# Optimization experiments

Measured on AMD Instinct MI355X. Metric: run time of the kernel, lower is better.

Reference implementation:

```python
import jax, jax.numpy as jnp
import numpy as np

USER_NUM = 50000
ITEM_NUM = 50000
N = USER_NUM + ITEM_NUM
VT_DIM = 512
CAT_NUM = 1000
CAT_DIM = 32
HIDDEN = 128
OUT = 64
E = 2_000_000
BAG = 5


def setup_inputs() -> dict:
    key = jax.random.key(0)
    ks = jax.random.split(key, 12)
    inp = {
        "vt_feature": jax.random.normal(ks[0], (ITEM_NUM, VT_DIM), jnp.float32),
        "cat_indices": jax.random.randint(ks[1], (ITEM_NUM * BAG,), 0, CAT_NUM),
        "cat_offsets": jnp.arange(ITEM_NUM) * BAG,
        "edge_index": jax.random.randint(ks[2], (2, E), 0, N),
        # learned parameters
        "cat_table": jax.random.normal(ks[3], (CAT_NUM, CAT_DIM), jnp.float32) * 0.1,
        "fuse_w": jax.random.normal(ks[4], (HIDDEN, VT_DIM + CAT_DIM), jnp.float32) * (1.0 / np.sqrt(VT_DIM + CAT_DIM)),
        "user": jax.random.normal(ks[5], (USER_NUM, HIDDEN), jnp.float32) * 0.1,
        "w1_l": jax.random.normal(ks[6], (HIDDEN, HIDDEN), jnp.float32) * (1.0 / np.sqrt(HIDDEN)),
        "b1": jnp.zeros((HIDDEN,), jnp.float32),
        "w1_r": jax.random.normal(ks[7], (HIDDEN, HIDDEN), jnp.float32) * (1.0 / np.sqrt(HIDDEN)),
        "w2_l": jax.random.normal(ks[8], (OUT, HIDDEN), jnp.float32) * (1.0 / np.sqrt(HIDDEN)),
        "b2": jnp.zeros((OUT,), jnp.float32),
        "w2_r": jax.random.normal(ks[9], (OUT, HIDDEN), jnp.float32) * (1.0 / np.sqrt(HIDDEN)),
    }
    return inp


def _embedding_bag_mean(table, indices, offsets, num_bags):
    # EmbeddingBag(mode='mean') with offsets: segment-mean of table lookups.
    pos = jnp.arange(indices.shape[0])
    seg = jnp.searchsorted(offsets, pos, side="right") - 1  # bag id per index
    sums = jax.ops.segment_sum(table[indices], seg, num_segments=num_bags)
    cnt = jax.ops.segment_sum(jnp.ones_like(pos, jnp.float32), seg, num_segments=num_bags)
    return sums / jnp.maximum(cnt, 1.0)[:, None]


def _sage_conv(x, edge_index, w_l, b_l, w_r):
    # PyG SAGEConv (aggr='mean'): lin_l(mean_{j->i} x_j) + lin_r(x_i)
    src, dst = edge_index[0], edge_index[1]
    agg = jax.ops.segment_sum(x[src], dst, num_segments=N)
    deg = jax.ops.segment_sum(jnp.ones((src.shape[0],), x.dtype), dst, num_segments=N)
    agg = agg / jnp.maximum(deg, 1.0)[:, None]
    return agg @ w_l.T + b_l + x @ w_r.T


def reference(vt_feature, cat_indices, cat_offsets, edge_index, cat_table,
              fuse_w, user, w1_l, b1, w1_r, w2_l, b2, w2_r):
    cat_emb = _embedding_bag_mean(cat_table, cat_indices, cat_offsets, ITEM_NUM)
    item_feat = jnp.concatenate([vt_feature, cat_emb], axis=1) @ fuse_w.T
    x0 = jnp.concatenate([user, item_feat], axis=0)  # [N, hidden]
    x1 = jax.nn.leaky_relu(_sage_conv(x0, edge_index, w1_l, b1, w1_r), negative_slope=0.01)
    # dropout is identity in eval mode
    x2 = _sage_conv(x1, edge_index, w2_l, b2, w2_r)
    return x2
```

## Files before the change

### kernel.cpp

```cpp
#include <hip/hip_runtime.h>

#define USER_N   50000
#define ITEM_N   50000
#define NNODE    100000
#define VT_DIM   512
#define CAT_DIM  32
#define HIDDEN   128
#define OUTD     64
#define PADCAP   64

#define BINC    8192
#define NBKT    98
#define BSHIFT  10
#define SLICES  8

typedef __attribute__((ext_vector_type(8))) short short8;
typedef __attribute__((ext_vector_type(4))) float f32x4;

__device__ __forceinline__ float bf2f(unsigned short u) {
    return __uint_as_float(((unsigned int)u) << 16);
}
__device__ __forceinline__ unsigned short f2bf(float f) {
    unsigned int u = __float_as_uint(f);
    unsigned int r = u + 0x7fffu + ((u >> 16) & 1u);
    return (unsigned short)(r >> 16);
}
__device__ __forceinline__ unsigned int pk2(float lo, float hi) {
    return ((unsigned int)f2bf(hi) << 16) | (unsigned int)f2bf(lo);
}
__device__ __forceinline__ void acc8(float* a, uint4 v) {
    a[0] += __uint_as_float(v.x << 16);
    a[1] += __uint_as_float(v.x & 0xffff0000u);
    a[2] += __uint_as_float(v.y << 16);
    a[3] += __uint_as_float(v.y & 0xffff0000u);
    a[4] += __uint_as_float(v.z << 16);
    a[5] += __uint_as_float(v.z & 0xffff0000u);
    a[6] += __uint_as_float(v.w << 16);
    a[7] += __uint_as_float(v.w & 0xffff0000u);
}
__device__ __forceinline__ void acc8w(float* a, uint4 v, float w) {
    a[0] += w * __uint_as_float(v.x << 16);
    a[1] += w * __uint_as_float(v.x & 0xffff0000u);
    a[2] += w * __uint_as_float(v.y << 16);
    a[3] += w * __uint_as_float(v.y & 0xffff0000u);
    a[4] += w * __uint_as_float(v.z << 16);
    a[5] += w * __uint_as_float(v.z & 0xffff0000u);
    a[6] += w * __uint_as_float(v.w << 16);
    a[7] += w * __uint_as_float(v.w & 0xffff0000u);
}

__global__ __launch_bounds__(256) void k_catemb(const float* __restrict__ cat_table,
                                                const int* __restrict__ cat_idx,
                                                const int* __restrict__ cat_off,
                                                unsigned short* __restrict__ catemb,
                                                int item_num, int total_idx) {
    int gid = blockIdx.x * 256 + threadIdx.x;
    int item = gid >> 5;
    int d = gid & 31;
    if (item >= item_num) return;
    int s = cat_off[item];
    int e = (item + 1 < item_num) ? cat_off[item + 1] : total_idx;
    float acc = 0.f;
    for (int j = s; j < e; ++j) {
        int idx = cat_idx[j];
        acc += cat_table[idx * CAT_DIM + d];
    }
    int cnt = e - s;
    float inv = 1.f / (float)(cnt > 0 ? cnt : 1);
    catemb[(size_t)item * CAT_DIM + d] = f2bf(acc * inv);
}

__global__ __launch_bounds__(256) void k_copy_user(const float* __restrict__ user,
                                                   unsigned short* __restrict__ x0, int n4) {
    int gid = blockIdx.x * 256 + threadIdx.x;
    if (gid >= n4) return;
    float4 v = ((const float4*)user)[gid];
    ushort4 o;
    o.x = f2bf(v.x); o.y = f2bf(v.y); o.z = f2bf(v.z); o.w = f2bf(v.w);
    ((ushort4*)x0)[gid] = o;
}

#define ASTR 40

__global__ __launch_bounds__(256, 4) void k_fuse_mfma(const float* __restrict__ vt,
                                                      const unsigned short* __restrict__ catemb,
                                                      const float* __restrict__ fw,
                                                      unsigned short* __restrict__ x0) {
    __shared__ __align__(16) unsigned short Al[64 * ASTR];
    __shared__ __align__(16) unsigned short Bl[128 * ASTR];
    int tid = threadIdx.x;
    int wave = tid >> 6, lane = tid & 63, quad = lane >> 4, l16 = lane & 15;
    int br0 = blockIdx.x * 64;
    int row = tid >> 2, q4 = tid & 3;
    int arow = br0 + row;

    f32x4 acc[8];
#pragma unroll
    for (int n = 0; n < 8; n++) acc[n] = (f32x4){0.f, 0.f, 0.f, 0.f};

    for (int kb = 0; kb < 17; ++kb) {
        if (kb < 16) {
            if (arow < ITEM_N) {
                const float* src = vt + (size_t)arow * VT_DIM + kb * 32 + q4 * 8;
                float4 v0 = ((const float4*)src)[0];
                float4 v1 = ((const float4*)src)[1];
                ushort4 o0, o1;
                o0.x = f2bf(v0.x); o0.y = f2bf(v0.y); o0.z = f2bf(v0.z); o0.w = f2bf(v0.w);
                o1.x = f2bf(v1.x); o1.y = f2bf(v1.y); o1.z = f2bf(v1.z); o1.w = f2bf(v1.w);
                *(ushort4*)&Al[row * ASTR + q4 * 8]     = o0;
                *(ushort4*)&Al[row * ASTR + q4 * 8 + 4] = o1;
            } else {
                ushort4 z = {0, 0, 0, 0};
                *(ushort4*)&Al[row * ASTR + q4 * 8]     = z;
                *(ushort4*)&Al[row * ASTR + q4 * 8 + 4] = z;
            }
        } else {
            if (arow < ITEM_N) {
                uint4 v = *(const uint4*)(catemb + (size_t)arow * CAT_DIM + q4 * 8);
                *(uint4*)&Al[row * ASTR + q4 * 8] = v;
            } else {
                uint4 z = {0, 0, 0, 0};
                *(uint4*)&Al[row * ASTR + q4 * 8] = z;
            }
        }
        {
            int n = tid & 127, kh = tid >> 7;
            const float* src = fw + (size_t)n * (VT_DIM + CAT_DIM) + kb * 32 + kh * 16;
#pragma unroll
            for (int i = 0; i < 4; i++) {
                float4 v = ((const float4*)src)[i];
                ushort4 o;
                o.x = f2bf(v.x); o.y = f2bf(v.y); o.z = f2bf(v.z); o.w = f2bf(v.w);
                *(ushort4*)&Bl[n * ASTR + kh * 16 + i * 4] = o;
            }
        }
        __syncthreads();
        short8 av = *(const short8*)&Al[(wave * 16 + l16) * ASTR + quad * 8];
#pragma unroll
        for (int nf = 0; nf < 8; nf++) {
            short8 bv = *(const short8*)&Bl[(nf * 16 + l16) * ASTR + quad * 8];
            acc[nf] = __builtin_amdgcn_mfma_f32_16x16x32_bf16(av, bv, acc[nf], 0, 0, 0);
        }
        __syncthreads();
    }
    int rbase = br0 + wave * 16 + quad * 4;
#pragma unroll
    for (int r = 0; r < 4; r++) {
        int orow = rbase + r;
        if (orow < ITEM_N) {
#pragma unroll
            for (int nf = 0; nf < 8; nf++) {
                int col = nf * 16 + l16;
                x0[(size_t)(USER_N + orow) * HIDDEN + col] = f2bf(acc[nf][r]);
            }
        }
    }
}

__global__ __launch_bounds__(256, 4) void k_l1_mfma(const unsigned short* __restrict__ agg1,
                                                    const unsigned short* __restrict__ x0,
                                                    const float* __restrict__ w1l,
                                                    const float* __restrict__ w1r,
                                                    const float* __restrict__ b1,
                                                    unsigned short* __restrict__ x1) {
    __shared__ __align__(16) unsigned short Al[64 * ASTR];
    __shared__ __align__(16) unsigned short Bl[128 * ASTR];
    int tid = threadIdx.x;
    int wave = tid >> 6, lane = tid & 63, quad = lane >> 4, l16 = lane & 15;
    int br0 = blockIdx.x * 64;
    int row = tid >> 2, q4 = tid & 3;
    int arow = br0 + row;

    f32x4 acc[8];
#pragma unroll
    for (int n = 0; n < 8; n++) acc[n] = (f32x4){0.f, 0.f, 0.f, 0.f};

    for (int kb = 0; kb < 8; ++kb) {
        const unsigned short* abase = (kb < 4) ? agg1 : x0;
        int kc = (kb & 3) * 32;
        if (arow < NNODE) {
            uint4 v = *(const uint4*)(abase + (size_t)arow * HIDDEN + kc + q4 * 8);
            *(uint4*)&Al[row * ASTR + q4 * 8] = v;
        } else {
            uint4 z = {0, 0, 0, 0};
            *(uint4*)&Al[row * ASTR + q4 * 8] = z;
        }
        {
            int n = tid & 127, kh = tid >> 7;
            const float* src = ((kb < 4) ? w1l : w1r) + (size_t)n * HIDDEN + kc + kh * 16;
#pragma unroll
            for (int i = 0; i < 4; i++) {
                float4 v = ((const float4*)src)[i];
                ushort4 o;
                o.x = f2bf(v.x); o.y = f2bf(v.y); o.z = f2bf(v.z); o.w = f2bf(v.w);
                *(ushort4*)&Bl[n * ASTR + kh * 16 + i * 4] = o;
            }
        }
        __syncthreads();
        short8 av = *(const short8*)&Al[(wave * 16 + l16) * ASTR + quad * 8];
#pragma unroll
        for (int nf = 0; nf < 8; nf++) {
            short8 bv = *(const short8*)&Bl[(nf * 16 + l16) * ASTR + quad * 8];
            acc[nf] = __builtin_amdgcn_mfma_f32_16x16x32_bf16(av, bv, acc[nf], 0, 0, 0);
        }
        __syncthreads();
    }
    float bias[8];
#pragma unroll
    for (int nf = 0; nf < 8; nf++) bias[nf] = b1[nf * 16 + l16];
    int rbase = br0 + wave * 16 + quad * 4;
#pragma unroll
    for (int r = 0; r < 4; r++) {
        int orow = rbase + r;
        if (orow < NNODE) {
#pragma unroll
            for (int nf = 0; nf < 8; nf++) {
                int col = nf * 16 + l16;
                float v = acc[nf][r] + bias[nf];
                v = (v >= 0.f) ? v : 0.01f * v;
                x1[(size_t)orow * HIDDEN + col] = f2bf(v);
            }
        }
    }
}

__global__ __launch_bounds__(256, 4) void k_l2_mfma(const unsigned short* __restrict__ x1,
                                                    const float* __restrict__ w2l,
                                                    const float* __restrict__ w2r,
                                                    const float* __restrict__ b2,
                                                    unsigned short* __restrict__ y1,
                                                    float* __restrict__ outw) {
    __shared__ __align__(16) unsigned short Al[64 * ASTR];
    __shared__ __align__(16) unsigned short Bl[128 * ASTR];
    int tid = threadIdx.x;
    int wave = tid >> 6, lane = tid & 63, quad = lane >> 4, l16 = lane & 15;
    int br0 = blockIdx.x * 64;
    int row = tid >> 2, q4 = tid & 3;
    int arow = br0 + row;

    f32x4 acc[8];
#pragma unroll
    for (int n = 0; n < 8; n++) acc[n] = (f32x4){0.f, 0.f, 0.f, 0.f};

    for (int kb = 0; kb < 4; ++kb) {
        int kc = kb * 32;
        if (arow < NNODE) {
            uint4 v = *(const uint4*)(x1 + (size_t)arow * HIDDEN + kc + q4 * 8);
            *(uint4*)&Al[row * ASTR + q4 * 8] = v;
        } else {
            uint4 z = {0, 0, 0, 0};
            *(uint4*)&Al[row * ASTR + q4 * 8] = z;
        }
        {
            int n = tid & 127, kh = tid >> 7;
            const float* wsrc = (n < 64) ? (w2l + (size_t)n * HIDDEN)
                                         : (w2r + (size_t)(n - 64) * HIDDEN);
            const float* src = wsrc + kc + kh * 16;
#pragma unroll
            for (int i = 0; i < 4; i++) {
                float4 v = ((const float4*)src)[i];
                ushort4 o;
                o.x = f2bf(v.x); o.y = f2bf(v.y); o.z = f2bf(v.z); o.w = f2bf(v.w);
                *(ushort4*)&Bl[n * ASTR + kh * 16 + i * 4] = o;
            }
        }
        __syncthreads();
        short8 av = *(const short8*)&Al[(wave * 16 + l16) * ASTR + quad * 8];
#pragma unroll
        for (int nf = 0; nf < 8; nf++) {
            short8 bv = *(const short8*)&Bl[(nf * 16 + l16) * ASTR + quad * 8];
            acc[nf] = __builtin_amdgcn_mfma_f32_16x16x32_bf16(av, bv, acc[nf], 0, 0, 0);
        }
        __syncthreads();
    }
    float bias2[4];
#pragma unroll
    for (int nf = 0; nf < 4; nf++) bias2[nf] = b2[nf * 16 + l16];
    int rbase = br0 + wave * 16 + quad * 4;
#pragma unroll
    for (int r = 0; r < 4; r++) {
        int orow = rbase + r;
        if (orow < NNODE) {
#pragma unroll
            for (int nf = 0; nf < 4; nf++) {
                int col = nf * 16 + l16;
                y1[(size_t)orow * OUTD + col] = f2bf(acc[nf][r]);
            }
#pragma unroll
            for (int nf = 4; nf < 8; nf++) {
                int col = (nf - 4) * 16 + l16;
                outw[(size_t)orow * OUTD + col] = acc[nf][r] + bias2[nf - 4];
            }
        }
    }
}

__global__ __launch_bounds__(256) void k_deg(const int* __restrict__ dst, int ne4, int ne, int* __restrict__ deg) {
    int t = blockIdx.x * 256 + threadIdx.x;
    int base = t * 4;
    if (t < ne4) {
        int4 d4 = *(const int4*)&dst[base];
        atomicAdd(&deg[d4.x], 1);
        atomicAdd(&deg[d4.y], 1);
        atomicAdd(&deg[d4.z], 1);
        atomicAdd(&deg[d4.w], 1);
    } else {
        for (int e = base; e < ne; ++e) atomicAdd(&deg[dst[e]], 1);
    }
}

__global__ __launch_bounds__(256) void k_scanA(const int* __restrict__ deg, int n, int* __restrict__ bsum) {
    __shared__ int sd[256];
    int i = blockIdx.x * 256 + threadIdx.x;
    sd[threadIdx.x] = (i < n) ? deg[i] : 0;
    __syncthreads();
    for (int o = 128; o > 0; o >>= 1) {
        if (threadIdx.x < o) sd[threadIdx.x] += sd[threadIdx.x + o];
        __syncthreads();
    }
    if (threadIdx.x == 0) bsum[blockIdx.x] = sd[0];
}

__global__ __launch_bounds__(512) void k_scanB(const int* __restrict__ bsum, int nb, int* __restrict__ boff) {
    __shared__ int sd[512];
    int t = threadIdx.x;
    int v = (t < nb) ? bsum[t] : 0;
    sd[t] = v;
    __syncthreads();
    for (int o = 1; o < 512; o <<= 1) {
        int x = 0;
        if (t >= o) x = sd[t - o];
        __syncthreads();
        sd[t] += x;
        __syncthreads();
    }
    if (t < nb) boff[t] = sd[t] - v;
}

__global__ __launch_bounds__(256) void k_scanC(const int* __restrict__ deg, int n,
                                               const int* __restrict__ boff,
                                               int* __restrict__ offs, int* __restrict__ cursor, int ne) {
    __shared__ int sd[256];
    int i = blockIdx.x * 256 + threadIdx.x;
    int v = (i < n) ? deg[i] : 0;
    sd[threadIdx.x] = v;
    __syncthreads();
    for (int o = 1; o < 256; o <<= 1) {
        int x = 0;
        if (threadIdx.x >= o) x = sd[threadIdx.x - o];
        __syncthreads();
        sd[threadIdx.x] += x;
        __syncthreads();
    }
    if (i < n) {
        int ex = boff[blockIdx.x] + sd[threadIdx.x] - v;
        offs[i] = ex;
        cursor[i] = ex;
    }
    if (i == 0) offs[n] = ne;
}

__global__ __launch_bounds__(256) void k_scatter(const int* __restrict__ src, const int* __restrict__ dst,
                                                 int ne4, int ne, int* __restrict__ cursor, int* __restrict__ csr) {
    int t = blockIdx.x * 256 + threadIdx.x;
    int base = t * 4;
    if (t < ne4) {
        int4 d4 = *(const int4*)&dst[base];
        int4 s4 = *(const int4*)&src[base];
        int p0 = atomicAdd(&cursor[d4.x], 1);
        int p1 = atomicAdd(&cursor[d4.y], 1);
        int p2 = atomicAdd(&cursor[d4.z], 1);
        int p3 = atomicAdd(&cursor[d4.w], 1);
        csr[p0] = s4.x;
        csr[p1] = s4.y;
        csr[p2] = s4.z;
        csr[p3] = s4.w;
    } else {
        for (int e = base; e < ne; ++e) {
            int slot = atomicAdd(&cursor[dst[e]], 1);
            csr[slot] = src[e];
        }
    }
}

__global__ __launch_bounds__(256) void k_scatter_pad(const int* __restrict__ src, const int* __restrict__ dst,
                                                     int ne4, int ne, int* __restrict__ cursor,
                                                     int* __restrict__ csrp) {
    int t = blockIdx.x * 256 + threadIdx.x;
    int base = t * 4;
    if (t < ne4) {
        int4 d4 = *(const int4*)&dst[base];
        int4 s4 = *(const int4*)&src[base];
        int p0 = atomicAdd(&cursor[d4.x], 1);
        int p1 = atomicAdd(&cursor[d4.y], 1);
        int p2 = atomicAdd(&cursor[d4.z], 1);
        int p3 = atomicAdd(&cursor[d4.w], 1);
        if (p0 < PADCAP) csrp[d4.x * PADCAP + p0] = s4.x;
        if (p1 < PADCAP) csrp[d4.y * PADCAP + p1] = s4.y;
        if (p2 < PADCAP) csrp[d4.z * PADCAP + p2] = s4.z;
        if (p3 < PADCAP) csrp[d4.w * PADCAP + p3] = s4.w;
    } else {
        for (int e = base; e < ne; ++e) {
            int d = dst[e];
            int slot = atomicAdd(&cursor[d], 1);
            if (slot < PADCAP) csrp[d * PADCAP + slot] = src[e];
        }
    }
}

__global__ __launch_bounds__(256) void k_hist(const int* __restrict__ dst, int ne,
                                              int nblk, int* __restrict__ hist) {
    __shared__ int lh[NBKT];
    int b = blockIdx.x;
    for (int i = threadIdx.x; i < NBKT; i += 256) lh[i] = 0;
    __syncthreads();
    int s = b * BINC;
    int e = (s + BINC < ne) ? (s + BINC) : ne;
    int nv = (e - s) & ~3;
    for (int j = s + threadIdx.x * 4; j < s + nv; j += 1024) {
        int4 d4 = *(const int4*)&dst[j];
        atomicAdd(&lh[d4.x >> BSHIFT], 1);
        atomicAdd(&lh[d4.y >> BSHIFT], 1);
        atomicAdd(&lh[d4.z >> BSHIFT], 1);
        atomicAdd(&lh[d4.w >> BSHIFT], 1);
    }
    for (int j = s + nv + threadIdx.x; j < e; j += 256) {
        atomicAdd(&lh[dst[j] >> BSHIFT], 1);
    }
    __syncthreads();
    for (int i = threadIdx.x; i < NBKT; i += 256) hist[i * nblk + b] = lh[i];
}

__global__ __launch_bounds__(1024) void k_scan1(int* __restrict__ hist, int tot) {
    __shared__ int ls[1024];
    int t = threadIdx.x;
    int K = (tot + 1023) >> 10;
    int base = t * K;
    int end = base + K;
    if (end > tot) end = tot;
    int s = 0;
    for (int i = base; i < end; ++i) s += hist[i];
    ls[t] = s;
    __syncthreads();
    for (int o = 1; o < 1024; o <<= 1) {
        int v = (t >= o) ? ls[t - o] : 0;
        __syncthreads();
        ls[t] += v;
        __syncthreads();
    }
    int run = ls[t] - s;
    for (int i = base; i < end; ++i) {
        int tmp = hist[i];
        hist[i] = run;
        run += tmp;
    }
}

__global__ __launch_bounds__(256) void k_binscatter(const int* __restrict__ src,
                                                    const int* __restrict__ dst,
                                                    int ne, int nblk,
                                                    const int* __restrict__ hist,
                                                    int2* __restrict__ ebin) {
    __shared__ int lc[NBKT];
    int b = blockIdx.x;
    for (int i = threadIdx.x; i < NBKT; i += 256) lc[i] = hist[i * nblk + b];
    __syncthreads();
    int s = b * BINC;
    int e = (s + BINC < ne) ? (s + BINC) : ne;
    int nv = (e - s) & ~3;
    for (int j = s + threadIdx.x * 4; j < s + nv; j += 1024) {
        int4 d4 = *(const int4*)&dst[j];
        int4 s4 = *(const int4*)&src[j];
        int p0 = atomicAdd(&lc[d4.x >> BSHIFT], 1);
        int p1 = atomicAdd(&lc[d4.y >> BSHIFT], 1);
        int p2 = atomicAdd(&lc[d4.z >> BSHIFT], 1);
        int p3 = atomicAdd(&lc[d4.w >> BSHIFT], 1);
        ebin[p0] = make_int2(s4.x, d4.x);
        ebin[p1] = make_int2(s4.y, d4.y);
        ebin[p2] = make_int2(s4.z, d4.z);
        ebin[p3] = make_int2(s4.w, d4.w);
    }
    for (int j = s + nv + threadIdx.x; j < e; j += 256) {
        int d = dst[j];
        int p = atomicAdd(&lc[d >> BSHIFT], 1);
        ebin[p] = make_int2(src[j], d);
    }
}

__global__ __launch_bounds__(256) void k_scatter_bkt(const int2* __restrict__ ebin,
                                                     const int* __restrict__ hist,
                                                     int nblk, int ne,
                                                     int* __restrict__ cursor,
                                                     int* __restrict__ csrp) {
    int xcd = blockIdx.x & 7;
    int w = blockIdx.x >> 3;
    int i = w / SLICES, sl = w - i * SLICES;
    int b = xcd + (i << 3);
    if (b >= NBKT) return;
    int s0 = hist[b * nblk];
    int e0 = (b + 1 < NBKT) ? hist[(b + 1) * nblk] : ne;
    int len = e0 - s0;
    int per = (len + SLICES - 1) / SLICES;
    int s = s0 + sl * per;
    int e = (s + per < e0) ? (s + per) : e0;
    for (int j = s + threadIdx.x; j < e; j += 256) {
        int2 p = ebin[j];
        int slot = atomicAdd(&cursor[p.y], 1);
        if (slot < PADCAP) csrp[p.y * PADCAP + slot] = p.x;
    }
}

__global__ __launch_bounds__(256) void k_agg1(const unsigned short* __restrict__ x0,
                                              const int* __restrict__ offs,
                                              const int* __restrict__ cnts,
                                              int pad,
                                              const int* __restrict__ csr,
                                              unsigned short* __restrict__ agg1) {
    int wid = (blockIdx.x << 2) + (threadIdx.x >> 6);
    if (wid >= NNODE) return;
    int lane = threadIdx.x & 63;
    int quad = lane >> 4;
    int l16 = lane & 15;
    int s, e, d;
    if (pad) {
        s = wid << 6;
        int c = cnts[wid];
        d = c;
        e = s + (c < PADCAP ? c : PADCAP);
    } else {
        s = offs[wid];
        e = offs[wid + 1];
        d = e - s;
    }
    float a[8];
#pragma unroll
    for (int i = 0; i < 8; i++) a[i] = 0.f;
    for (int j = s; j < e; j += 32) {
        int sn[8];
        float w[8];
#pragma unroll
        for (int t = 0; t < 8; t++) {
            int myj = j + 4 * t + quad;
            bool ok = (myj < e);
            sn[t] = ok ? csr[myj] : csr[s];
            w[t] = ok ? 1.f : 0.f;
        }
        uint4 v[8];
#pragma unroll
        for (int t = 0; t < 8; t++)
            v[t] = *(const uint4*)&x0[(size_t)sn[t] * HIDDEN + l16 * 8];
#pragma unroll
        for (int t = 0; t < 8; t++) acc8w(a, v[t], w[t]);
    }
#pragma unroll
    for (int i = 0; i < 8; i++) {
        a[i] += __shfl_xor(a[i], 16, 64);
        a[i] += __shfl_xor(a[i], 32, 64);
    }
    float inv = 1.f / (float)(d > 0 ? d : 1);
    if (quad == 0) {
        uint4 o;
        o.x = pk2(a[0] * inv, a[1] * inv);
        o.y = pk2(a[2] * inv, a[3] * inv);
        o.z = pk2(a[4] * inv, a[5] * inv);
        o.w = pk2(a[6] * inv, a[7] * inv);
        *(uint4*)&agg1[(size_t)wid * HIDDEN + l16 * 8] = o;
    }
}

__global__ __launch_bounds__(256) void k_agg2_out(const unsigned short* __restrict__ y1,
                                                  const int* __restrict__ offs,
                                                  const int* __restrict__ cnts,
                                                  int pad,
                                                  const int* __restrict__ csr,
                                                  float* __restrict__ out) {
    int wid = (blockIdx.x << 2) + (threadIdx.x >> 6);
    if (wid >= NNODE) return;
    int lane = threadIdx.x & 63;
    int oct = lane >> 3;
    int l8 = lane & 7;
    int s, e, d;
    if (pad) {
        s = wid << 6;
        int c = cnts[wid];
        d = c;
        e = s + (c < PADCAP ? c : PADCAP);
    } else {
        s = offs[wid];
        e = offs[wid + 1];
        d = e - s;
    }
    float a[8];
#pragma unroll
    for (int i = 0; i < 8; i++) a[i] = 0.f;
    for (int j = s; j < e; j += 64) {
        int sn[8];
        float w[8];
#pragma unroll
        for (int t = 0; t < 8; t++) {
            int myj = j + 8 * t + oct;
            bool ok = (myj < e);
            sn[t] = ok ? csr[myj] : csr[s];
            w[t] = ok ? 1.f : 0.f;
        }
        uint4 v[8];
#pragma unroll
        for (int t = 0; t < 8; t++)
            v[t] = *(const uint4*)&y1[(size_t)sn[t] * OUTD + l8 * 8];
#pragma unroll
        for (int t = 0; t < 8; t++) acc8w(a, v[t], w[t]);
    }
#pragma unroll
    for (int i = 0; i < 8; i++) {
        a[i] += __shfl_xor(a[i], 8, 64);
        a[i] += __shfl_xor(a[i], 16, 64);
        a[i] += __shfl_xor(a[i], 32, 64);
    }
    float inv = 1.f / (float)(d > 0 ? d : 1);
    if (oct == 0) {
        float4* op = (float4*)&out[(size_t)wid * OUTD + l8 * 8];
        float4 p0 = op[0];
        float4 p1 = op[1];
        float4 o0, o1;
        o0.x = a[0] * inv + p0.x; o0.y = a[1] * inv + p0.y;
        o0.z = a[2] * inv + p0.z; o0.w = a[3] * inv + p0.w;
        o1.x = a[4] * inv + p1.x; o1.y = a[5] * inv + p1.y;
        o1.z = a[6] * inv + p1.z; o1.w = a[7] * inv + p1.w;
        op[0] = o0;
        op[1] = o1;
    }
}

extern "C" void kernel_launch(void* const* d_in, const int* in_sizes, int n_in,
                              void* d_out, int out_size, void* d_ws, size_t ws_size,
                              hipStream_t stream) {
    const float* vt      = (const float*)d_in[0];
    const int*   cat_idx = (const int*)d_in[1];
    const int*   cat_off = (const int*)d_in[2];
    const int*   ei      = (const int*)d_in[3];
    const float* cat_tab = (const float*)d_in[4];
    const float* fuse_w  = (const float*)d_in[5];
    const float* user    = (const float*)d_in[6];
    const float* w1l     = (const float*)d_in[7];
    const float* b1      = (const float*)d_in[8];
    const float* w1r     = (const float*)d_in[9];
    const float* w2l     = (const float*)d_in[10];
    const float* b2      = (const float*)d_in[11];
    const float* w2r     = (const float*)d_in[12];
    float* out = (float*)d_out;

    const int ne = in_sizes[3] / 2;
    const int ne4 = ne / 4;
    const int total_idx = in_sizes[1];
    const int* esrc = ei;
    const int* edst = ei + ne;

    const size_t SZ_X0  = (size_t)NNODE * HIDDEN * 2;
    const size_t SZ_PAD = (size_t)NNODE * PADCAP * 4;
    const size_t SZ_CSR = (size_t)ne * 4;
    const size_t SZ_INT = (size_t)NNODE * 4;

    size_t need_pad = SZ_X0 * 3 + SZ_PAD + SZ_INT + 8192;
    size_t need_csr = SZ_X0 * 3 + SZ_CSR + SZ_INT * 3 + 4 * 4096 + 4096;

    char* p = (char*)d_ws;
    auto alloc = [&](size_t bytes) {
        char* q = p;
        p += (bytes + 255) & ~(size_t)255;
        return q;
    };

    const int nscan = (NNODE + 255) / 256;
    const int sc_blocks = (ne4 + 255) / 256;

    if (ws_size >= need_pad) {
        unsigned short* x0   = (unsigned short*)alloc(SZ_X0);
        unsigned short* aggY = (unsigned short*)alloc(SZ_X0);
        unsigned short* x1   = (unsigned short*)alloc(SZ_X0);
        int*            csrp = (int*)alloc(SZ_PAD);
        int*          cursor = (int*)alloc(SZ_INT);
        unsigned short* catemb = (unsigned short*)csrp;

        k_catemb<<<(ITEM_N * 32 + 255) / 256, 256, 0, stream>>>(cat_tab, cat_idx, cat_off, catemb, ITEM_N, total_idx);
        k_copy_user<<<(USER_N * HIDDEN / 4 + 255) / 256, 256, 0, stream>>>(user, x0, USER_N * HIDDEN / 4);
        k_fuse_mfma<<<(ITEM_N + 63) / 64, 256, 0, stream>>>(vt, catemb, fuse_w, x0);

        hipMemsetAsync(cursor, 0, SZ_INT, stream);

        const int nblk = (ne + BINC - 1) / BINC;
        bool fast_bin = ((size_t)ne * sizeof(int2) <= SZ_X0) &&
                        ((size_t)NBKT * nblk * sizeof(int) <= SZ_X0);
        if (fast_bin) {
            int*  hist = (int*)aggY;
            int2* ebin = (int2*)x1;
            k_hist<<<nblk, 256, 0, stream>>>(edst, ne, nblk, hist);
            k_scan1<<<1, 1024, 0, stream>>>(hist, NBKT * nblk);
            k_binscatter<<<nblk, 256, 0, stream>>>(esrc, edst, ne, nblk, hist, ebin);
            k_scatter_bkt<<<8 * 13 * SLICES, 256, 0, stream>>>(ebin, hist, nblk, ne, cursor, csrp);
        } else {
            k_scatter_pad<<<sc_blocks, 256, 0, stream>>>(esrc, edst, ne4, ne, cursor, csrp);
        }

        k_agg1<<<(NNODE + 3) / 4, 256, 0, stream>>>(x0, cursor, cursor, 1, csrp, aggY);
        k_l1_mfma<<<(NNODE + 63) / 64, 256, 0, stream>>>(aggY, x0, w1l, w1r, b1, x1);
        k_l2_mfma<<<(NNODE + 63) / 64, 256, 0, stream>>>(x1, w2l, w2r, b2, aggY, out);
        k_agg2_out<<<(NNODE + 3) / 4, 256, 0, stream>>>(aggY, cursor, cursor, 1, csrp, out);
    } else if (ws_size >= need_csr) {
        unsigned short* x0   = (unsigned short*)alloc(SZ_X0);
        unsigned short* aggY = (unsigned short*)alloc(SZ_X0);
        unsigned short* x1   = (unsigned short*)alloc(SZ_X0);
        char*           R4   = (char*)alloc(SZ_CSR);
        int* deg    = (int*)alloc(SZ_INT);
        int* offs   = (int*)alloc(SZ_INT + 256);
        int* cursor = (int*)alloc(SZ_INT);
        int* bsum   = (int*)alloc(512 * 4);
        int* boff   = (int*)alloc(512 * 4);
        unsigned short* catemb = (unsigned short*)R4;
        int*            csr    = (int*)R4;

        k_catemb<<<(ITEM_N * 32 + 255) / 256, 256, 0, stream>>>(cat_tab, cat_idx, cat_off, catemb, ITEM_N, total_idx);
        k_copy_user<<<(USER_N * HIDDEN / 4 + 255) / 256, 256, 0, stream>>>(user, x0, USER_N * HIDDEN / 4);
        k_fuse_mfma<<<(ITEM_N + 63) / 64, 256, 0, stream>>>(vt, catemb, fuse_w, x0);

        hipMemsetAsync(deg, 0, SZ_INT, stream);
        k_deg<<<sc_blocks, 256, 0, stream>>>(edst, ne4, ne, deg);
        k_scanA<<<nscan, 256, 0, stream>>>(deg, NNODE, bsum);
        k_scanB<<<1, 512, 0, stream>>>(bsum, nscan, boff);
        k_scanC<<<nscan, 256, 0, stream>>>(deg, NNODE, boff, offs, cursor, ne);
        k_scatter<<<sc_blocks, 256, 0, stream>>>(esrc, edst, ne4, ne, cursor, csr);

        k_agg1<<<(NNODE + 3) / 4, 256, 0, stream>>>(x0, offs, offs, 0, csr, aggY);
        k_l1_mfma<<<(NNODE + 63) / 64, 256, 0, stream>>>(aggY, x0, w1l, w1r, b1, x1);
        k_l2_mfma<<<(NNODE + 63) / 64, 256, 0, stream>>>(x1, w2l, w2r, b2, aggY, out);
        k_agg2_out<<<(NNODE + 3) / 4, 256, 0, stream>>>(aggY, offs, offs, 0, csr, out);
    } else {
        hipMemsetAsync(d_out, 0, (size_t)out_size * 4, stream);
    }
}
```

Baseline: 538.5 us.

## Pre-convert weights to bf16 and load MFMA operands directly with register double-buffering

Adds a kernel that converts all weight matrices to bf16 once per call, so the GEMM kernels no longer reconvert the fp32 weights in every block. The three MFMA GEMM kernels drop their LDS staging and __syncthreads and have each lane load its A/B fragments straight from global memory (L2-resident weights), double-buffered in registers across k-steps. The cost is extra register pressure and redundant per-wave weight loads from L2/global in place of shared LDS reuse across the four waves.

```diff
diff --git a/kernel.cpp b/kernel.cpp
--- a/kernel.cpp
+++ b/kernel.cpp
@@ -14,6 +14,11 @@
 #define BSHIFT  10
 #define SLICES  8
 
+#define FW_E  (128 * 544)
+#define W1_E  (128 * 128)
+#define W2_E  (64 * 128)
+#define WB_E  (FW_E + 2 * W1_E + 2 * W2_E)
+
 typedef __attribute__((ext_vector_type(8))) short short8;
 typedef __attribute__((ext_vector_type(4))) float f32x4;
 
@@ -27,6 +32,12 @@
 }
 __device__ __forceinline__ unsigned int pk2(float lo, float hi) {
     return ((unsigned int)f2bf(hi) << 16) | (unsigned int)f2bf(lo);
+}
+__device__ __forceinline__ short8 cvt8(float4 a, float4 b) {
+    union { unsigned short u[8]; short8 s; } r;
+    r.u[0] = f2bf(a.x); r.u[1] = f2bf(a.y); r.u[2] = f2bf(a.z); r.u[3] = f2bf(a.w);
+    r.u[4] = f2bf(b.x); r.u[5] = f2bf(b.y); r.u[6] = f2bf(b.z); r.u[7] = f2bf(b.w);
+    return r.s;
 }
 __device__ __forceinline__ void acc8(float* a, uint4 v) {
     a[0] += __uint_as_float(v.x << 16);
@@ -47,6 +58,27 @@
     a[5] += w * __uint_as_float(v.z & 0xffff0000u);
     a[6] += w * __uint_as_float(v.w << 16);
     a[7] += w * __uint_as_float(v.w & 0xffff0000u);
+}
+
+__global__ __launch_bounds__(256) void k_prepw(const float* __restrict__ fw,
+                                               const float* __restrict__ w1l,
+                                               const float* __restrict__ w1r,
+                                               const float* __restrict__ w2l,
+                                               const float* __restrict__ w2r,
+                                               unsigned short* __restrict__ wb) {
+    int i4 = (blockIdx.x * 256 + threadIdx.x) * 4;
+    if (i4 >= WB_E) return;
+    const float* src;
+    int off;
+    if (i4 < FW_E)                    { src = fw;  off = i4; }
+    else if (i4 < FW_E + W1_E)        { src = w1l; off = i4 - FW_E; }
+    else if (i4 < FW_E + 2 * W1_E)    { src = w1r; off = i4 - FW_E - W1_E; }
+    else if (i4 < FW_E + 2*W1_E+W2_E) { src = w2l; off = i4 - FW_E - 2 * W1_E; }
+    else                              { src = w2r; off = i4 - FW_E - 2 * W1_E - W2_E; }
+    float4 v = *(const float4*)&src[off];
+    ushort4 o;
+    o.x = f2bf(v.x); o.y = f2bf(v.y); o.z = f2bf(v.z); o.w = f2bf(v.w);
+    *(ushort4*)&wb[i4] = o;
 }
 
 __global__ __launch_bounds__(256) void k_catemb(const float* __restrict__ cat_table,
@@ -80,70 +112,63 @@
     ((ushort4*)x0)[gid] = o;
 }
 
-#define ASTR 40
 
 __global__ __launch_bounds__(256, 4) void k_fuse_mfma(const float* __restrict__ vt,
                                                       const unsigned short* __restrict__ catemb,
-                                                      const float* __restrict__ fw,
+                                                      const unsigned short* __restrict__ fwb,
                                                       unsigned short* __restrict__ x0) {
-    __shared__ __align__(16) unsigned short Al[64 * ASTR];
-    __shared__ __align__(16) unsigned short Bl[128 * ASTR];
     int tid = threadIdx.x;
     int wave = tid >> 6, lane = tid & 63, quad = lane >> 4, l16 = lane & 15;
-    int br0 = blockIdx.x * 64;
-    int row = tid >> 2, q4 = tid & 3;
-    int arow = br0 + row;
+    int r0 = blockIdx.x * 64 + wave * 16;
+    int arow = r0 + l16;
+    int lrow = (arow < ITEM_N) ? arow : (ITEM_N - 1);
+    const float* vrow = vt + (size_t)lrow * VT_DIM + quad * 8;
+    const unsigned short* crow = catemb + (size_t)lrow * CAT_DIM + quad * 8;
+    const unsigned short* bb = fwb + quad * 8 + (size_t)l16 * (VT_DIM + CAT_DIM);
 
     f32x4 acc[8];
 #pragma unroll
     for (int n = 0; n < 8; n++) acc[n] = (f32x4){0.f, 0.f, 0.f, 0.f};
 
+    short8 A0, A1;
+    short8 B0[8], B1[8];
+
+#define FUSE_LD(kb, A, B)                                                        \
+    do {                                                                         \
+        if ((kb) < 16) {                                                         \
+            float4 v0 = *(const float4*)(vrow + (kb) * 32);                      \
+            float4 v1 = *(const float4*)(vrow + (kb) * 32 + 4);                  \
+            A = cvt8(v0, v1);                                                    \
+        } else {                                                                 \
+            A = *(const short8*)crow;                                            \
+        }                                                                        \
+        _Pragma("unroll")                                                        \
+        for (int nf = 0; nf < 8; nf++)                                           \
+            B[nf] = *(const short8*)(bb + (kb) * 32 + (size_t)nf * 16 * (VT_DIM + CAT_DIM)); \
+    } while (0)
+
+#define FUSE_MF(A, B)                                                            \
+    do {                                                                         \
+        _Pragma("unroll")                                                        \
+        for (int nf = 0; nf < 8; nf++)                                           \
+            acc[nf] = __builtin_amdgcn_mfma_f32_16x16x32_bf16(A, B[nf], acc[nf], 0, 0, 0); \
+    } while (0)
+
+    FUSE_LD(0, A0, B0);
+#pragma unroll
     for (int kb = 0; kb < 17; ++kb) {
-        if (kb < 16) {
-            if (arow < ITEM_N) {
-                const float* src = vt + (size_t)arow * VT_DIM + kb * 32 + q4 * 8;
-                float4 v0 = ((const float4*)src)[0];
-                float4 v1 = ((const float4*)src)[1];
-                ushort4 o0, o1;
-                o0.x = f2bf(v0.x); o0.y = f2bf(v0.y); o0.z = f2bf(v0.z); o0.w = f2bf(v0.w);
-                o1.x = f2bf(v1.x); o1.y = f2bf(v1.y); o1.z = f2bf(v1.z); o1.w = f2bf(v1.w);
-                *(ushort4*)&Al[row * ASTR + q4 * 8]     = o0;
-                *(ushort4*)&Al[row * ASTR + q4 * 8 + 4] = o1;
-            } else {
-                ushort4 z = {0, 0, 0, 0};
-                *(ushort4*)&Al[row * ASTR + q4 * 8]     = z;
-                *(ushort4*)&Al[row * ASTR + q4 * 8 + 4] = z;
-            }
+        if ((kb & 1) == 0) {
+            if (kb + 1 < 17) FUSE_LD(kb + 1, A1, B1);
+            FUSE_MF(A0, B0);
         } else {
-            if (arow < ITEM_N) {
-                uint4 v = *(const uint4*)(catemb + (size_t)arow * CAT_DIM + q4 * 8);
-                *(uint4*)&Al[row * ASTR + q4 * 8] = v;
-            } else {
-                uint4 z = {0, 0, 0, 0};
-                *(uint4*)&Al[row * ASTR + q4 * 8] = z;
-            }
-        }
-        {
-            int n = tid & 127, kh = tid >> 7;
-            const float* src = fw + (size_t)n * (VT_DIM + CAT_DIM) + kb * 32 + kh * 16;
-#pragma unroll
-            for (int i = 0; i < 4; i++) {
-                float4 v = ((const float4*)src)[i];
-                ushort4 o;
-                o.x = f2bf(v.x); o.y = f2bf(v.y); o.z = f2bf(v.z); o.w = f2bf(v.w);
-                *(ushort4*)&Bl[n * ASTR + kh * 16 + i * 4] = o;
-            }
-        }
-        __syncthreads();
-        short8 av = *(const short8*)&Al[(wave * 16 + l16) * ASTR + quad * 8];
-#pragma unroll
-        for (int nf = 0; nf < 8; nf++) {
-            short8 bv = *(const short8*)&Bl[(nf * 16 + l16) * ASTR + quad * 8];
-            acc[nf] = __builtin_amdgcn_mfma_f32_16x16x32_bf16(av, bv, acc[nf], 0, 0, 0);
-        }
-        __syncthreads();
-    }
-    int rbase = br0 + wave * 16 + quad * 4;
+            if (kb + 1 < 17) FUSE_LD(kb + 1, A0, B0);
+            FUSE_MF(A1, B1);
+        }
+    }
+#undef FUSE_LD
+#undef FUSE_MF
+
+    int rbase = r0 + quad * 4;
 #pragma unroll
     for (int r = 0; r < 4; r++) {
         int orow = rbase + r;
@@ -159,56 +184,62 @@
 
 __global__ __launch_bounds__(256, 4) void k_l1_mfma(const unsigned short* __restrict__ agg1,
                                                     const unsigned short* __restrict__ x0,
-                                                    const float* __restrict__ w1l,
-                                                    const float* __restrict__ w1r,
+                                                    const unsigned short* __restrict__ w1lb,
+                                                    const unsigned short* __restrict__ w1rb,
                                                     const float* __restrict__ b1,
                                                     unsigned short* __restrict__ x1) {
-    __shared__ __align__(16) unsigned short Al[64 * ASTR];
-    __shared__ __align__(16) unsigned short Bl[128 * ASTR];
     int tid = threadIdx.x;
     int wave = tid >> 6, lane = tid & 63, quad = lane >> 4, l16 = lane & 15;
-    int br0 = blockIdx.x * 64;
-    int row = tid >> 2, q4 = tid & 3;
-    int arow = br0 + row;
+    int r0 = blockIdx.x * 64 + wave * 16;
+    int arow = r0 + l16;
+    int lrow = (arow < NNODE) ? arow : (NNODE - 1);
+    const unsigned short* ag = agg1 + (size_t)lrow * HIDDEN + quad * 8;
+    const unsigned short* xs = x0 + (size_t)lrow * HIDDEN + quad * 8;
+    const unsigned short* bl = w1lb + quad * 8 + (size_t)l16 * HIDDEN;
+    const unsigned short* br = w1rb + quad * 8 + (size_t)l16 * HIDDEN;
 
     f32x4 acc[8];
 #pragma unroll
     for (int n = 0; n < 8; n++) acc[n] = (f32x4){0.f, 0.f, 0.f, 0.f};
 
+    short8 A0, A1;
+    short8 B0[8], B1[8];
+
+#define L1_LD(kb, A, B)                                                          \
+    do {                                                                         \
+        A = ((kb) < 4) ? *(const short8*)(ag + ((kb) & 3) * 32)                  \
+                       : *(const short8*)(xs + ((kb) & 3) * 32);                 \
+        const unsigned short* wbase = ((kb) < 4) ? bl : br;                      \
+        _Pragma("unroll")                                                        \
+        for (int nf = 0; nf < 8; nf++)                                           \
+            B[nf] = *(const short8*)(wbase + ((kb) & 3) * 32 + (size_t)nf * 16 * HIDDEN); \
+    } while (0)
+
+#define L1_MF(A, B)                                                              \
+    do {                                                                         \
+        _Pragma("unroll")                                                        \
+        for (int nf = 0; nf < 8; nf++)                                           \
+            acc[nf] = __builtin_amdgcn_mfma_f32_16x16x32_bf16(A, B[nf], acc[nf], 0, 0, 0); \
+    } while (0)
+
+    L1_LD(0, A0, B0);
+#pragma unroll
     for (int kb = 0; kb < 8; ++kb) {
-        const unsigned short* abase = (kb < 4) ? agg1 : x0;
-        int kc = (kb & 3) * 32;
-        if (arow < NNODE) {
-            uint4 v = *(const uint4*)(abase + (size_t)arow * HIDDEN + kc + q4 * 8);
-            *(uint4*)&Al[row * ASTR + q4 * 8] = v;
+        if ((kb & 1) == 0) {
+            if (kb + 1 < 8) L1_LD(kb + 1, A1, B1);
+            L1_MF(A0, B0);
         } else {
-            uint4 z = {0, 0, 0, 0};
-            *(uint4*)&Al[row * ASTR + q4 * 8] = z;
-        }
-        {
-            int n = tid & 127, kh = tid >> 7;
-            const float* src = ((kb < 4) ? w1l : w1r) + (size_t)n * HIDDEN + kc + kh * 16;
-#pragma unroll
-            for (int i = 0; i < 4; i++) {
-                float4 v = ((const float4*)src)[i];
-                ushort4 o;
-                o.x = f2bf(v.x); o.y = f2bf(v.y); o.z = f2bf(v.z); o.w = f2bf(v.w);
-                *(ushort4*)&Bl[n * ASTR + kh * 16 + i * 4] = o;
-            }
-        }
-        __syncthreads();
-        short8 av = *(const short8*)&Al[(wave * 16 + l16) * ASTR + quad * 8];
-#pragma unroll
-        for (int nf = 0; nf < 8; nf++) {
-            short8 bv = *(const short8*)&Bl[(nf * 16 + l16) * ASTR + quad * 8];
-            acc[nf] = __builtin_amdgcn_mfma_f32_16x16x32_bf16(av, bv, acc[nf], 0, 0, 0);
-        }
-        __syncthreads();
-    }
+            if (kb + 1 < 8) L1_LD(kb + 1, A0, B0);
+            L1_MF(A1, B1);
+        }
+    }
+#undef L1_LD
+#undef L1_MF
+
     float bias[8];
 #pragma unroll
     for (int nf = 0; nf < 8; nf++) bias[nf] = b1[nf * 16 + l16];
-    int rbase = br0 + wave * 16 + quad * 4;
+    int rbase = r0 + quad * 4;
 #pragma unroll
     for (int r = 0; r < 4; r++) {
         int orow = rbase + r;
@@ -225,58 +256,63 @@
 }
 
 __global__ __launch_bounds__(256, 4) void k_l2_mfma(const unsigned short* __restrict__ x1,
-                                                    const float* __restrict__ w2l,
-                                                    const float* __restrict__ w2r,
+                                                    const unsigned short* __restrict__ w2lb,
+                                                    const unsigned short* __restrict__ w2rb,
                                                     const float* __restrict__ b2,
                                                     unsigned short* __restrict__ y1,
                                                     float* __restrict__ outw) {
-    __shared__ __align__(16) unsigned short Al[64 * ASTR];
-    __shared__ __align__(16) unsigned short Bl[128 * ASTR];
     int tid = threadIdx.x;
     int wave = tid >> 6, lane = tid & 63, quad = lane >> 4, l16 = lane & 15;
-    int br0 = blockIdx.x * 64;
-    int row = tid >> 2, q4 = tid & 3;
-    int arow = br0 + row;
+    int r0 = blockIdx.x * 64 + wave * 16;
+    int arow = r0 + l16;
+    int lrow = (arow < NNODE) ? arow : (NNODE - 1);
+    const unsigned short* xs = x1 + (size_t)lrow * HIDDEN + quad * 8;
+    const unsigned short* bl = w2lb + quad * 8 + (size_t)l16 * HIDDEN;
+    const unsigned short* br = w2rb + quad * 8 + (size_t)l16 * HIDDEN;
 
     f32x4 acc[8];
 #pragma unroll
     for (int n = 0; n < 8; n++) acc[n] = (f32x4){0.f, 0.f, 0.f, 0.f};
 
+    short8 A0, A1;
+    short8 B0[8], B1[8];
+
+#define L2_LD(kb, A, B)                                                          \
+    do {                                                                         \
+        A = *(const short8*)(xs + (kb) * 32);                                    \
+        _Pragma("unroll")                                                        \
+        for (int nf = 0; nf < 4; nf++)                                           \
+            B[nf] = *(const short8*)(bl + (kb) * 32 + (size_t)nf * 16 * HIDDEN); \
+        _Pragma("unroll")                                                        \
+        for (int nf = 4; nf < 8; nf++)                                           \
+            B[nf] = *(const short8*)(br + (kb) * 32 + (size_t)(nf - 4) * 16 * HIDDEN); \
+    } while (0)
+
+#define L2_MF(A, B)                                                              \
+    do {                                                                         \
+        _Pragma("unroll")                                                        \
+        for (int nf = 0; nf < 8; nf++)                                           \
+            acc[nf] = __builtin_amdgcn_mfma_f32_16x16x32_bf16(A, B[nf], acc[nf], 0, 0, 0); \
+    } while (0)
+
+    L2_LD(0, A0, B0);
+#pragma unroll
     for (int kb = 0; kb < 4; ++kb) {
-        int kc = kb * 32;
-        if (arow < NNODE) {
-            uint4 v = *(const uint4*)(x1 + (size_t)arow * HIDDEN + kc + q4 * 8);
-            *(uint4*)&Al[row * ASTR + q4 * 8] = v;
+        if ((kb & 1) == 0) {
+            if (kb + 1 < 4) L2_LD(kb + 1, A1, B1);
+            L2_MF(A0, B0);
         } else {
-            uint4 z = {0, 0, 0, 0};
-            *(uint4*)&Al[row * ASTR + q4 * 8] = z;
-        }
-        {
-            int n = tid & 127, kh = tid >> 7;
-            const float* wsrc = (n < 64) ? (w2l + (size_t)n * HIDDEN)
-                                         : (w2r + (size_t)(n - 64) * HIDDEN);
-            const float* src = wsrc + kc + kh * 16;
-#pragma unroll
-            for (int i = 0; i < 4; i++) {
-                float4 v = ((const float4*)src)[i];
-                ushort4 o;
-                o.x = f2bf(v.x); o.y = f2bf(v.y); o.z = f2bf(v.z); o.w = f2bf(v.w);
-                *(ushort4*)&Bl[n * ASTR + kh * 16 + i * 4] = o;
-            }
-        }
-        __syncthreads();
-        short8 av = *(const short8*)&Al[(wave * 16 + l16) * ASTR + quad * 8];
-#pragma unroll
-        for (int nf = 0; nf < 8; nf++) {
-            short8 bv = *(const short8*)&Bl[(nf * 16 + l16) * ASTR + quad * 8];
-            acc[nf] = __builtin_amdgcn_mfma_f32_16x16x32_bf16(av, bv, acc[nf], 0, 0, 0);
-        }
-        __syncthreads();
-    }
+            if (kb + 1 < 4) L2_LD(kb + 1, A0, B0);
+            L2_MF(A1, B1);
+        }
+    }
+#undef L2_LD
+#undef L2_MF
+
     float bias2[4];
 #pragma unroll
     for (int nf = 0; nf < 4; nf++) bias2[nf] = b2[nf * 16 + l16];
-    int rbase = br0 + wave * 16 + quad * 4;
+    int rbase = r0 + quad * 4;
 #pragma unroll
     for (int r = 0; r < 4; r++) {
         int orow = rbase + r;
@@ -659,9 +695,10 @@
     const size_t SZ_PAD = (size_t)NNODE * PADCAP * 4;
     const size_t SZ_CSR = (size_t)ne * 4;
     const size_t SZ_INT = (size_t)NNODE * 4;
-
-    size_t need_pad = SZ_X0 * 3 + SZ_PAD + SZ_INT + 8192;
-    size_t need_csr = SZ_X0 * 3 + SZ_CSR + SZ_INT * 3 + 4 * 4096 + 4096;
+    const size_t SZ_WB  = (size_t)WB_E * 2;
+
+    size_t need_pad = SZ_WB + SZ_X0 * 3 + SZ_PAD + SZ_INT + 8192;
+    size_t need_csr = SZ_WB + SZ_X0 * 3 + SZ_CSR + SZ_INT * 3 + 4 * 4096 + 4096;
 
     char* p = (char*)d_ws;
     auto alloc = [&](size_t bytes) {
@@ -674,6 +711,7 @@
     const int sc_blocks = (ne4 + 255) / 256;
 
     if (ws_size >= need_pad) {
+        unsigned short* wb   = (unsigned short*)alloc(SZ_WB);
         unsigned short* x0   = (unsigned short*)alloc(SZ_X0);
         unsigned short* aggY = (unsigned short*)alloc(SZ_X0);
         unsigned short* x1   = (unsigned short*)alloc(SZ_X0);
@@ -681,9 +719,16 @@
         int*          cursor = (int*)alloc(SZ_INT);
         unsigned short* catemb = (unsigned short*)csrp;
 
+        unsigned short* fwb  = wb;
+        unsigned short* w1lb = wb + FW_E;
+        unsigned short* w1rb = w1lb + W1_E;
+        unsigned short* w2lb = w1rb + W1_E;
+        unsigned short* w2rb = w2lb + W2_E;
+
+        k_prepw<<<(WB_E / 4 + 255) / 256, 256, 0, stream>>>(fuse_w, w1l, w1r, w2l, w2r, wb);
         k_catemb<<<(ITEM_N * 32 + 255) / 256, 256, 0, stream>>>(cat_tab, cat_idx, cat_off, catemb, ITEM_N, total_idx);
         k_copy_user<<<(USER_N * HIDDEN / 4 + 255) / 256, 256, 0, stream>>>(user, x0, USER_N * HIDDEN / 4);
-        k_fuse_mfma<<<(ITEM_N + 63) / 64, 256, 0, stream>>>(vt, catemb, fuse_w, x0);
+        k_fuse_mfma<<<(ITEM_N + 63) / 64, 256, 0, stream>>>(vt, catemb, fwb, x0);
 
         hipMemsetAsync(cursor, 0, SZ_INT, stream);
 
@@ -702,10 +747,11 @@
         }
 
         k_agg1<<<(NNODE + 3) / 4, 256, 0, stream>>>(x0, cursor, cursor, 1, csrp, aggY);
-        k_l1_mfma<<<(NNODE + 63) / 64, 256, 0, stream>>>(aggY, x0, w1l, w1r, b1, x1);
-        k_l2_mfma<<<(NNODE + 63) / 64, 256, 0, stream>>>(x1, w2l, w2r, b2, aggY, out);
+        k_l1_mfma<<<(NNODE + 63) / 64, 256, 0, stream>>>(aggY, x0, w1lb, w1rb, b1, x1);
+        k_l2_mfma<<<(NNODE + 63) / 64, 256, 0, stream>>>(x1, w2lb, w2rb, b2, aggY, out);
         k_agg2_out<<<(NNODE + 3) / 4, 256, 0, stream>>>(aggY, cursor, cursor, 1, csrp, out);
     } else if (ws_size >= need_csr) {
+        unsigned short* wb   = (unsigned short*)alloc(SZ_WB);
         unsigned short* x0   = (unsigned short*)alloc(SZ_X0);
         unsigned short* aggY = (unsigned short*)alloc(SZ_X0);
         unsigned short* x1   = (unsigned short*)alloc(SZ_X0);
@@ -718,9 +764,16 @@
         unsigned short* catemb = (unsigned short*)R4;
         int*            csr    = (int*)R4;
 
+        unsigned short* fwb  = wb;
+        unsigned short* w1lb = wb + FW_E;
+        unsigned short* w1rb = w1lb + W1_E;
+        unsigned short* w2lb = w1rb + W1_E;
+        unsigned short* w2rb = w2lb + W2_E;
+
+        k_prepw<<<(WB_E / 4 + 255) / 256, 256, 0, stream>>>(fuse_w, w1l, w1r, w2l, w2r, wb);
         k_catemb<<<(ITEM_N * 32 + 255) / 256, 256, 0, stream>>>(cat_tab, cat_idx, cat_off, catemb, ITEM_N, total_idx);
         k_copy_user<<<(USER_N * HIDDEN / 4 + 255) / 256, 256, 0, stream>>>(user, x0, USER_N * HIDDEN / 4);
-        k_fuse_mfma<<<(ITEM_N + 63) / 64, 256, 0, stream>>>(vt, catemb, fuse_w, x0);
+        k_fuse_mfma<<<(ITEM_N + 63) / 64, 256, 0, stream>>>(vt, catemb, fwb, x0);
 
         hipMemsetAsync(deg, 0, SZ_INT, stream);
         k_deg<<<sc_blocks, 256, 0, stream>>>(edst, ne4, ne, deg);
@@ -730,8 +783,8 @@
         k_scatter<<<sc_blocks, 256, 0, stream>>>(esrc, edst, ne4, ne, cursor, csr);
 
         k_agg1<<<(NNODE + 3) / 4, 256, 0, stream>>>(x0, offs, offs, 0, csr, aggY);
-        k_l1_mfma<<<(NNODE + 63) / 64, 256, 0, stream>>>(aggY, x0, w1l, w1r, b1, x1);
-        k_l2_mfma<<<(NNODE + 63) / 64, 256, 0, stream>>>(x1, w2l, w2r, b2, aggY, out);
+        k_l1_mfma<<<(NNODE + 63) / 64, 256, 0, stream>>>(aggY, x0, w1lb, w1rb, b1, x1);
+        k_l2_mfma<<<(NNODE + 63) / 64, 256, 0, stream>>>(x1, w2lb, w2rb, b2, aggY, out);
         k_agg2_out<<<(NNODE + 3) / 4, 256, 0, stream>>>(aggY, offs, offs, 0, csr, out);
     } else {
         hipMemsetAsync(d_out, 0, (size_t)out_size * 4, stream);
```

Measured after the change: 574.0 us. 6.6% more time.
